# Optimization experiments

Measured on AMD Instinct MI355X. Metric: run time of the kernel, lower is better.

Reference implementation:

```python
import jax, jax.numpy as jnp
import numpy as np

B, K, F_DIM, H_DIM, HEADS = 512, 17, 256, 256, 4
N = B * K           # 8704 flattened nodes
E = 139264          # edges (avg degree 16)
NEG_SLOPE = 0.2


def setup_inputs() -> dict:
    key = jax.random.key(0)
    ks = jax.random.split(key, 12)
    s_in = 1.0 / np.sqrt(F_DIM)
    s_hid = 1.0 / np.sqrt(H_DIM)
    return {
        "kpt_feature": jax.random.normal(ks[0], (B, K, F_DIM), jnp.float32),
        "edge_index": jax.random.randint(ks[1], (2, E), 0, N, jnp.int64),
        # conv1: F_DIM -> HEADS x H_DIM, concat=False (mean)
        "W1": jax.random.normal(ks[2], (F_DIM, HEADS * H_DIM), jnp.float32) * s_in,
        "a_src1": jax.random.normal(ks[3], (HEADS, H_DIM), jnp.float32) * s_hid,
        "a_dst1": jax.random.normal(ks[4], (HEADS, H_DIM), jnp.float32) * s_hid,
        "b1": jnp.zeros((H_DIM,), jnp.float32),
        # conv2: H_DIM -> HEADS x F_DIM, concat=False (mean)
        "W2": jax.random.normal(ks[5], (H_DIM, HEADS * F_DIM), jnp.float32) * s_hid,
        "a_src2": jax.random.normal(ks[6], (HEADS, F_DIM), jnp.float32) * s_in,
        "a_dst2": jax.random.normal(ks[7], (HEADS, F_DIM), jnp.float32) * s_in,
        "b2": jnp.zeros((F_DIM,), jnp.float32),
    }


def gat_conv(x, src, dst, W, a_src, a_dst, bias):
    # x: [N, Fin]; src/dst: [E'] (self-loops included); W: [Fin, H*C]
    n = x.shape[0]
    heads, c = a_src.shape
    h = (x @ W).reshape(n, heads, c)                       # [N,H,C]
    alpha_src = jnp.einsum("nhc,hc->nh", h, a_src)         # [N,H]
    alpha_dst = jnp.einsum("nhc,hc->nh", h, a_dst)
    e = jax.nn.leaky_relu(alpha_src[src] + alpha_dst[dst], NEG_SLOPE)  # [E',H]
    # segment softmax over incoming edges of each destination node
    emax = jax.ops.segment_max(e, dst, num_segments=n)
    emax = jnp.where(jnp.isfinite(emax), emax, 0.0)
    ex = jnp.exp(e - emax[dst])
    denom = jax.ops.segment_sum(ex, dst, num_segments=n)
    alpha = ex / denom[dst]                                # [E',H]
    msg = alpha[:, :, None] * h[src]                       # [E',H,C]
    out = jax.ops.segment_sum(msg, dst, num_segments=n)    # [N,H,C]
    return out.mean(axis=1) + bias                         # concat=False -> mean


def reference(kpt_feature, edge_index, W1, a_src1, a_dst1, b1, W2, a_src2, a_dst2, b2):
    b, k, f = kpt_feature.shape
    n = b * k
    x = kpt_feature.reshape(n, f)
    loop = jnp.arange(n, dtype=edge_index.dtype)
    src = jnp.concatenate([edge_index[0], loop])  # PyG add_self_loops=True
    dst = jnp.concatenate([edge_index[1], loop])
    x = gat_conv(x, src, dst, W1, a_src1, a_dst1, b1)
    x = jax.nn.relu(x)
    x = gat_conv(x, src, dst, W2, a_src2, a_dst2, b2)
    return x.reshape(b, k, f)
```

## Files before the change

kernel.cpp:

```cpp
#include <hip/hip_runtime.h>
#include <hip/hip_fp16.h>
#include <math.h>

#define NNODES 8704
#define NEDGE  139264
#define EPLUS  (NEDGE + NNODES)
#define NEG_SLOPE 0.2f
#define DEGCAP 64
#define LDSK   40

#define NB_PV  16
#define NB_WC  512
#define NB_SC  ((EPLUS + 255) / 256)
#define NB_AL  (NNODES / 4)

typedef _Float16 f16x8 __attribute__((ext_vector_type(8)));
typedef _Float16 f16x4 __attribute__((ext_vector_type(4)));
typedef float    f32x4 __attribute__((ext_vector_type(4)));

__device__ __forceinline__ float lrelu(float v) { return v >= 0.f ? v : NEG_SLOPE * v; }

__global__ __launch_bounds__(256) void prep_all(const float* __restrict__ W1,
                                                const float* __restrict__ as1,
                                                const float* __restrict__ ad1,
                                                const float* __restrict__ W2,
                                                const float* __restrict__ as2,
                                                const float* __restrict__ ad2,
                                                float* __restrict__ pbuf,
                                                int* __restrict__ cnt,
                                                float* __restrict__ alphasB,
                                                _Float16* __restrict__ Wc1,
                                                _Float16* __restrict__ Wc2) {
    __shared__ float tile[32][33];
    const int b = blockIdx.x;
    const int t = threadIdx.x;
    if (b < NB_PV) {
        for (int i = b * 256 + t; i < NNODES; i += NB_PV * 256) cnt[i] = 0;
        for (int i = b * 256 + t; i < NNODES * 8; i += NB_PV * 256) alphasB[i] = 0.f;
        float* a_sh = &tile[0][0];
        const int layer = b >> 3, sd = (b >> 2) & 1, h = b & 3;
        const float* W  = layer ? W2 : W1;
        const float* av = layer ? (sd ? ad2 : as2) : (sd ? ad1 : as1);
        a_sh[t] = av[h * 256 + t];
        __syncthreads();
        float acc = 0.f;
        const float* Wr = W + (size_t)t * 1024 + h * 256;
#pragma unroll 8
        for (int c = 0; c < 256; ++c) acc += Wr[c] * a_sh[c];
        pbuf[b * 256 + t] = acc;
    } else {
        const int idx = b - NB_PV;
        const int k0 = (idx & 7) * 32, o0 = ((idx >> 3) & 7) * 32;
        const int z = idx >> 6;
        const int layer = z >> 2, h = z & 3;
        const float* W = layer ? W2 : W1;
        _Float16* Wc   = layer ? Wc2 : Wc1;
#pragma unroll
        for (int p = 0; p < 4; ++p) {
            int e = t + p * 256; int kk = e >> 5, oo = e & 31;
            tile[kk][oo] = W[(size_t)(k0 + kk) * 1024 + h * 256 + o0 + oo];
        }
        __syncthreads();
#pragma unroll
        for (int p = 0; p < 4; ++p) {
            int e = t + p * 256; int oo = e >> 5, kk = e & 31;
            Wc[(size_t)(o0 + oo) * 1024 + h * 256 + k0 + kk] = (_Float16)tile[kk][oo];
        }
    }
}

__global__ __launch_bounds__(256) void scatter_alpha(const int* __restrict__ ei,
                                                     int* __restrict__ cnt,
                                                     int* __restrict__ csr,
                                                     const float* __restrict__ xf,
                                                     _Float16* __restrict__ xh_out,
                                                     const float* __restrict__ p ,
                                                     float* __restrict__ asrc,
                                                     float* __restrict__ adst) {
    const int b = blockIdx.x;
    const int t = threadIdx.x;
    if (b < NB_SC) {
        int e = b * 256 + t;
        if (e >= EPLUS) return;
        int src, dst;
        if (e < NEDGE) { src = ei[e]; dst = ei[NEDGE + e]; }
        else           { src = dst = e - NEDGE; }
        int slot = atomicAdd(&cnt[dst], 1);
        if (slot < DEGCAP) csr[dst * DEGCAP + slot] = src;
    } else {
        const int wave = t >> 6, l = t & 63;
        const int n = (b - NB_SC) * 4 + wave;
        float4 pv[8];
#pragma unroll
        for (int v = 0; v < 8; ++v) pv[v] = *(const float4*)(p + v * 256 + l * 4);
        float4 xv = *(const float4*)(xf + (size_t)n * 256 + l * 4);
        f16x4 hv = {(_Float16)xv.x, (_Float16)xv.y, (_Float16)xv.z, (_Float16)xv.w};
        *(f16x4*)(xh_out + (size_t)n * 256 + l * 4) = hv;
        float d[8];
#pragma unroll
        for (int v = 0; v < 8; ++v)
            d[v] = xv.x * pv[v].x + xv.y * pv[v].y + xv.z * pv[v].z + xv.w * pv[v].w;
#pragma unroll
        for (int off = 1; off <= 32; off <<= 1)
#pragma unroll
            for (int v = 0; v < 8; ++v) d[v] += __shfl_xor(d[v], off);
        if (l == 0) {
            *(float4*)(asrc + n * 4) = make_float4(d[0], d[1], d[2], d[3]);
            *(float4*)(adst + n * 4) = make_float4(d[4], d[5], d[6], d[7]);
        }
    }
}

__global__ __launch_bounds__(256) void agg_gather(const _Float16* __restrict__ xh,
                                                  const int* __restrict__ cnt,
                                                  const int* __restrict__ csr,
                                                  const float* __restrict__ asrc,
                                                  const float* __restrict__ adst,
                                                  _Float16* __restrict__ y) {
    const int w = threadIdx.x >> 6, l = threadIdx.x & 63;
    const int n = blockIdx.x * 4 + w;
    int deg = cnt[n]; if (deg > DEGCAP) deg = DEGCAP;

    float4 ad = *(const float4*)(adst + n * 4);
    int src_l = 0;
    float w0 = 0.f, w1 = 0.f, w2 = 0.f, w3 = 0.f;
    if (l < deg) {
        src_l = csr[n * DEGCAP + l];
        float4 as = *(const float4*)(asrc + src_l * 4);
        w0 = __expf(lrelu(as.x + ad.x));
        w1 = __expf(lrelu(as.y + ad.y));
        w2 = __expf(lrelu(as.z + ad.z));
        w3 = __expf(lrelu(as.w + ad.w));
    }
    float d0 = w0, d1 = w1, d2 = w2, d3 = w3;
#pragma unroll
    for (int off = 32; off >= 1; off >>= 1) {
        d0 += __shfl_xor(d0, off);
        d1 += __shfl_xor(d1, off);
        d2 += __shfl_xor(d2, off);
        d3 += __shfl_xor(d3, off);
    }
    w0 /= d0; w1 /= d1; w2 /= d2; w3 /= d3;

    float acc[4][4] = {};
    for (int s = 0; s < deg; ++s) {
        int src = __shfl(src_l, s);
        float u0 = __shfl(w0, s), u1 = __shfl(w1, s);
        float u2 = __shfl(w2, s), u3 = __shfl(w3, s);
        f16x4 xv = *(const f16x4*)(xh + (size_t)src * 256 + l * 4);
#pragma unroll
        for (int j = 0; j < 4; ++j) {
            float v = (float)xv[j];
            acc[j][0] += u0 * v; acc[j][1] += u1 * v;
            acc[j][2] += u2 * v; acc[j][3] += u3 * v;
        }
    }
#pragma unroll
    for (int h = 0; h < 4; ++h) {
        f16x4 pv = {(_Float16)acc[0][h], (_Float16)acc[1][h],
                    (_Float16)acc[2][h], (_Float16)acc[3][h]};
        *(f16x4*)(y + (size_t)n * 1024 + h * 256 + l * 4) = pv;
    }
}

__global__ __launch_bounds__(256) void gemm_out(const _Float16* __restrict__ Y,
                                                const _Float16* __restrict__ Wcatt,
                                                const float* __restrict__ bias,
                                                const float* __restrict__ p2,
                                                _Float16* __restrict__ outH,
                                                float* __restrict__ outF,
                                                float* __restrict__ asrc2,
                                                float* __restrict__ adst2) {
    __shared__ __align__(16) _Float16 As[2][64 * LDSK];
    __shared__ __align__(16) _Float16 Bs[2][128 * LDSK];
    __shared__ float p2s[8 * 128];
    const int t    = threadIdx.x;
    const int lane = t & 63;
    const int wave = t >> 6;
    const int wwr = wave >> 1, wwc = wave & 1;
    const int bm = blockIdx.x * 64;
    const int bn = blockIdx.y * 128;
    const int l15 = lane & 15, kb = lane >> 4;

    const int ar = t >> 2, ag = t & 3;

    if (p2) {
#pragma unroll
        for (int p = 0; p < 4; ++p) {
            int e = t + p * 256;
            p2s[e] = p2[(e >> 7) * 256 + bn + (e & 127)];
        }
    }

    {
        f16x8 va = *(const f16x8*)(Y + (size_t)(bm + ar) * 1024 + ag * 8);
        *(f16x8*)(&As[0][ar * LDSK + ag * 8]) = va;
#pragma unroll
        for (int p = 0; p < 2; ++p) {
            int e = t + p * 256;
            int row = e >> 2, g = e & 3;
            f16x8 vb = *(const f16x8*)(Wcatt + (size_t)(bn + row) * 1024 + g * 8);
            *(f16x8*)(&Bs[0][row * LDSK + g * 8]) = vb;
        }
    }
    __syncthreads();

    f32x4 acc[2][4] = {};
    int a_off[2], b_off[4];
#pragma unroll
    for (int i = 0; i < 2; ++i) a_off[i] = (wwr * 32 + i * 16 + l15) * LDSK + kb * 8;
#pragma unroll
    for (int j = 0; j < 4; ++j) b_off[j] = (wwc * 64 + j * 16 + l15) * LDSK + kb * 8;

    int cur = 0;
    for (int s = 0; s < 32; ++s) {
        f16x8 pa; f16x8 pb[2];
        if (s < 31) {
            int k0n = (s + 1) * 32;
            pa = *(const f16x8*)(Y + (size_t)(bm + ar) * 1024 + k0n + ag * 8);
#pragma unroll
            for (int p = 0; p < 2; ++p) {
                int e = t + p * 256;
                int row = e >> 2, g = e & 3;
                pb[p] = *(const f16x8*)(Wcatt + (size_t)(bn + row) * 1024 + k0n + g * 8);
            }
        }
        f16x8 af[2], bf[4];
#pragma unroll
        for (int i = 0; i < 2; ++i) af[i] = *(const f16x8*)(&As[cur][a_off[i]]);
#pragma unroll
        for (int j = 0; j < 4; ++j) bf[j] = *(const f16x8*)(&Bs[cur][b_off[j]]);
#pragma unroll
        for (int i = 0; i < 2; ++i)
#pragma unroll
            for (int j = 0; j < 4; ++j)
                acc[i][j] = __builtin_amdgcn_mfma_f32_16x16x32_f16(af[i], bf[j], acc[i][j], 0, 0, 0);
        if (s < 31) {
            *(f16x8*)(&As[cur ^ 1][ar * LDSK + ag * 8]) = pa;
#pragma unroll
            for (int p = 0; p < 2; ++p) {
                int e = t + p * 256;
                int row = e >> 2, g = e & 3;
                *(f16x8*)(&Bs[cur ^ 1][row * LDSK + g * 8]) = pb[p];
            }
        }
        __syncthreads();
        cur ^= 1;
    }

#pragma unroll
    for (int i = 0; i < 2; ++i)
#pragma unroll
        for (int q = 0; q < 4; ++q) {
            int row = bm + wwr * 32 + i * 16 + kb * 4 + q;
            float rv[4];
#pragma unroll
            for (int j = 0; j < 4; ++j) {
                int cl = wwc * 64 + j * 16 + l15;
                float r = 0.25f * acc[i][j][q] + bias[bn + cl];
                rv[j] = r;
                if (outH) outH[(size_t)row * 256 + bn + cl] = (_Float16)fmaxf(r, 0.f);
                else      outF[(size_t)row * 256 + bn + cl] = r;
            }
            if (p2) {
#pragma unroll
                for (int v = 0; v < 8; ++v) {
                    float ps = 0.f;
#pragma unroll
                    for (int j = 0; j < 4; ++j) {
                        int cl = wwc * 64 + j * 16 + l15;
                        ps += fmaxf(rv[j], 0.f) * p2s[v * 128 + cl];
                    }
#pragma unroll
                    for (int off = 1; off <= 8; off <<= 1) ps += __shfl_xor(ps, off);
                    if (l15 == 0) {
                        if (v < 4) atomicAdd(&asrc2[row * 4 + v], ps);
                        else       atomicAdd(&adst2[row * 4 + (v - 4)], ps);
                    }
                }
            }
        }
}

extern "C" void kernel_launch(void* const* d_in, const int* in_sizes, int n_in,
                              void* d_out, int out_size, void* d_ws, size_t ws_size,
                              hipStream_t stream) {
    const float* x0  = (const float*)d_in[0];
    const int*   ei  = (const int*)d_in[1];
    const float* W1  = (const float*)d_in[2];
    const float* as1 = (const float*)d_in[3];
    const float* ad1 = (const float*)d_in[4];
    const float* b1  = (const float*)d_in[5];
    const float* W2  = (const float*)d_in[6];
    const float* as2 = (const float*)d_in[7];
    const float* ad2 = (const float*)d_in[8];
    const float* b2  = (const float*)d_in[9];
    float* out = (float*)d_out;

    char* w = (char*)d_ws;
    _Float16* y   = (_Float16*)w; w += (size_t)NNODES * 1024 * 2;
    _Float16* x0h = (_Float16*)w; w += (size_t)NNODES * 256 * 2;
    _Float16* x1h = (_Float16*)w; w += (size_t)NNODES * 256 * 2;
    _Float16* Wc1 = (_Float16*)w; w += (size_t)256 * 1024 * 2;
    _Float16* Wc2 = (_Float16*)w; w += (size_t)256 * 1024 * 2;
    float* pbuf   = (float*)w;    w += 16 * 256 * 4;
    float* asrcA  = (float*)w;    w += NNODES * 4 * 4;
    float* adstA  = (float*)w;    w += NNODES * 4 * 4;
    float* alphasB = (float*)w;   w += NNODES * 8 * 4;
    float* asrcB  = alphasB;
    float* adstB  = alphasB + NNODES * 4;
    int* cnt      = (int*)w;      w += NNODES * 4;
    int* csr      = (int*)w;      w += (size_t)NNODES * DEGCAP * 4;

    const dim3 gemm_grid(NNODES / 64, 2);

    prep_all<<<NB_PV + NB_WC, 256, 0, stream>>>(W1, as1, ad1, W2, as2, ad2,
                                                pbuf, cnt, alphasB, Wc1, Wc2);
    scatter_alpha<<<NB_SC + NB_AL, 256, 0, stream>>>(ei, cnt, csr, x0, x0h, pbuf, asrcA, adstA);

    agg_gather<<<NNODES / 4, 256, 0, stream>>>(x0h, cnt, csr, asrcA, adstA, y);
    gemm_out<<<gemm_grid, 256, 0, stream>>>(y, Wc1, b1, pbuf + 8 * 256, x1h, nullptr, asrcB, adstB);

    agg_gather<<<NNODES / 4, 256, 0, stream>>>(x1h, cnt, csr, asrcB, adstB, y);
    gemm_out<<<gemm_grid, 256, 0, stream>>>(y, Wc2, b2, nullptr, nullptr, out, nullptr, nullptr);
}
```

Before: 132.0 us.

## Prefetch neighbor rows in aggregation and deepen GEMM global-load pipeline

```diff
diff --git a/kernel.cpp b/kernel.cpp
--- a/kernel.cpp
+++ b/kernel.cpp
@@ -142,18 +142,38 @@
     }
     w0 /= d0; w1 /= d1; w2 /= d2; w3 /= d3;
 
+    const _Float16* xbase = xh + l * 4;
     float acc[4][4] = {};
-    for (int s = 0; s < deg; ++s) {
-        int src = __shfl(src_l, s);
-        float u0 = __shfl(w0, s), u1 = __shfl(w1, s);
-        float u2 = __shfl(w2, s), u3 = __shfl(w3, s);
-        f16x4 xv = *(const f16x4*)(xh + (size_t)src * 256 + l * 4);
-#pragma unroll
-        for (int j = 0; j < 4; ++j) {
-            float v = (float)xv[j];
-            acc[j][0] += u0 * v; acc[j][1] += u1 * v;
-            acc[j][2] += u2 * v; acc[j][3] += u3 * v;
-        }
+    f16x4 xb[8], xn[8];
+#pragma unroll
+    for (int j = 0; j < 8; ++j) {
+        int src = __shfl(src_l, j);
+        if (j < deg) xb[j] = *(const f16x4*)(xbase + (size_t)src * 256);
+    }
+    for (int base = 0; base < deg; base += 8) {
+#pragma unroll
+        for (int j = 0; j < 8; ++j) {
+            int s = base + 8 + j;
+            int src = __shfl(src_l, s & 63);
+            if (s < deg) xn[j] = *(const f16x4*)(xbase + (size_t)src * 256);
+        }
+#pragma unroll
+        for (int j = 0; j < 8; ++j) {
+            int s = base + j;
+            if (s < deg) {
+                float u0 = __shfl(w0, s), u1 = __shfl(w1, s);
+                float u2 = __shfl(w2, s), u3 = __shfl(w3, s);
+                f16x4 xv = xb[j];
+#pragma unroll
+                for (int c = 0; c < 4; ++c) {
+                    float v = (float)xv[c];
+                    acc[c][0] += u0 * v; acc[c][1] += u1 * v;
+                    acc[c][2] += u2 * v; acc[c][3] += u3 * v;
+                }
+            }
+        }
+#pragma unroll
+        for (int j = 0; j < 8; ++j) xb[j] = xn[j];
     }
 #pragma unroll
     for (int h = 0; h < 4; ++h) {
@@ -183,6 +203,12 @@
     const int l15 = lane & 15, kb = lane >> 4;
 
     const int ar = t >> 2, ag = t & 3;
+    const int br0 = t >> 2, br1 = 64 + (t >> 2), bg = t & 3;
+    const _Float16* Yb  = Y     + (size_t)(bm + ar) * 1024 + ag * 8;
+    const _Float16* Wb0 = Wcatt + (size_t)(bn + br0) * 1024 + bg * 8;
+    const _Float16* Wb1 = Wcatt + (size_t)(bn + br1) * 1024 + bg * 8;
+    const int aw = ar * LDSK + ag * 8;
+    const int bw0 = br0 * LDSK + bg * 8, bw1 = br1 * LDSK + bg * 8;
 
     if (p2) {
 #pragma unroll
@@ -193,16 +219,17 @@
     }
 
     {
-        f16x8 va = *(const f16x8*)(Y + (size_t)(bm + ar) * 1024 + ag * 8);
-        *(f16x8*)(&As[0][ar * LDSK + ag * 8]) = va;
-#pragma unroll
-        for (int p = 0; p < 2; ++p) {
-            int e = t + p * 256;
-            int row = e >> 2, g = e & 3;
-            f16x8 vb = *(const f16x8*)(Wcatt + (size_t)(bn + row) * 1024 + g * 8);
-            *(f16x8*)(&Bs[0][row * LDSK + g * 8]) = vb;
-        }
-    }
+        f16x8 a0 = *(const f16x8*)(Yb);
+        f16x8 b0 = *(const f16x8*)(Wb0);
+        f16x8 b1 = *(const f16x8*)(Wb1);
+        *(f16x8*)(&As[0][aw])  = a0;
+        *(f16x8*)(&Bs[0][bw0]) = b0;
+        *(f16x8*)(&Bs[0][bw1]) = b1;
+    }
+    f16x8 a_s0 = *(const f16x8*)(Yb + 32);
+    f16x8 bb_s0[2] = { *(const f16x8*)(Wb0 + 32), *(const f16x8*)(Wb1 + 32) };
+    f16x8 a_s1 = *(const f16x8*)(Yb + 64);
+    f16x8 bb_s1[2] = { *(const f16x8*)(Wb0 + 64), *(const f16x8*)(Wb1 + 64) };
     __syncthreads();
 
     f32x4 acc[2][4] = {};
@@ -212,40 +239,53 @@
 #pragma unroll
     for (int j = 0; j < 4; ++j) b_off[j] = (wwc * 64 + j * 16 + l15) * LDSK + kb * 8;
 
-    int cur = 0;
-    for (int s = 0; s < 32; ++s) {
-        f16x8 pa; f16x8 pb[2];
-        if (s < 31) {
-            int k0n = (s + 1) * 32;
-            pa = *(const f16x8*)(Y + (size_t)(bm + ar) * 1024 + k0n + ag * 8);
-#pragma unroll
-            for (int p = 0; p < 2; ++p) {
-                int e = t + p * 256;
-                int row = e >> 2, g = e & 3;
-                pb[p] = *(const f16x8*)(Wcatt + (size_t)(bn + row) * 1024 + k0n + g * 8);
-            }
-        }
-        f16x8 af[2], bf[4];
-#pragma unroll
-        for (int i = 0; i < 2; ++i) af[i] = *(const f16x8*)(&As[cur][a_off[i]]);
-#pragma unroll
-        for (int j = 0; j < 4; ++j) bf[j] = *(const f16x8*)(&Bs[cur][b_off[j]]);
-#pragma unroll
-        for (int i = 0; i < 2; ++i)
-#pragma unroll
-            for (int j = 0; j < 4; ++j)
-                acc[i][j] = __builtin_amdgcn_mfma_f32_16x16x32_f16(af[i], bf[j], acc[i][j], 0, 0, 0);
-        if (s < 31) {
-            *(f16x8*)(&As[cur ^ 1][ar * LDSK + ag * 8]) = pa;
-#pragma unroll
-            for (int p = 0; p < 2; ++p) {
-                int e = t + p * 256;
-                int row = e >> 2, g = e & 3;
-                *(f16x8*)(&Bs[cur ^ 1][row * LDSK + g * 8]) = pb[p];
-            }
-        }
-        __syncthreads();
-        cur ^= 1;
+    for (int h = 0; h < 32; h += 2) {
+        {
+            f16x8 af[2], bf[4];
+#pragma unroll
+            for (int i = 0; i < 2; ++i) af[i] = *(const f16x8*)(&As[0][a_off[i]]);
+#pragma unroll
+            for (int j = 0; j < 4; ++j) bf[j] = *(const f16x8*)(&Bs[0][b_off[j]]);
+#pragma unroll
+            for (int i = 0; i < 2; ++i)
+#pragma unroll
+                for (int j = 0; j < 4; ++j)
+                    acc[i][j] = __builtin_amdgcn_mfma_f32_16x16x32_f16(af[i], bf[j], acc[i][j], 0, 0, 0);
+            *(f16x8*)(&As[1][aw])  = a_s0;
+            *(f16x8*)(&Bs[1][bw0]) = bb_s0[0];
+            *(f16x8*)(&Bs[1][bw1]) = bb_s0[1];
+            if (h + 3 < 32) {
+                int k = (h + 3) * 32;
+                a_s0 = *(const f16x8*)(Yb + k);
+                bb_s0[0] = *(const f16x8*)(Wb0 + k);
+                bb_s0[1] = *(const f16x8*)(Wb1 + k);
+            }
+            __syncthreads();
+        }
+        {
+            f16x8 af[2], bf[4];
+#pragma unroll
+            for (int i = 0; i < 2; ++i) af[i] = *(const f16x8*)(&As[1][a_off[i]]);
+#pragma unroll
+            for (int j = 0; j < 4; ++j) bf[j] = *(const f16x8*)(&Bs[1][b_off[j]]);
+#pragma unroll
+            for (int i = 0; i < 2; ++i)
+#pragma unroll
+                for (int j = 0; j < 4; ++j)
+                    acc[i][j] = __builtin_amdgcn_mfma_f32_16x16x32_f16(af[i], bf[j], acc[i][j], 0, 0, 0);
+            if (h + 2 < 32) {
+                *(f16x8*)(&As[0][aw])  = a_s1;
+                *(f16x8*)(&Bs[0][bw0]) = bb_s1[0];
+                *(f16x8*)(&Bs[0][bw1]) = bb_s1[1];
+            }
+            if (h + 4 < 32) {
+                int k = (h + 4) * 32;
+                a_s1 = *(const f16x8*)(Yb + k);
+                bb_s1[0] = *(const f16x8*)(Wb0 + k);
+                bb_s1[1] = *(const f16x8*)(Wb1 + k);
+            }
+            __syncthreads();
+        }
     }
 
 #pragma unroll
```

After: 123.8 us. 6.2% less time.
